# Kernel tuning notes

Hardware: AMD Instinct MI355X
Metric: run time of the kernel (lower is better)

The kernel has to match this reference:

```python
import jax, jax.numpy as jnp
import numpy as np
import math

B, N, D, H, E, EDGE_DIM, GEO_DIM = 32, 256, 512, 8, 1024, 256, 64
HD = D // H

def _lin(x, W, b):
    return x @ W.T + b

def _ln(x, g, b):
    m = x.mean(-1, keepdims=True)
    v = ((x - m) ** 2).mean(-1, keepdims=True)
    return (x - m) * jax.lax.rsqrt(v + 1e-5) * g + b

def setup_inputs() -> dict:
    key = jax.random.key(0)
    ks = jax.random.split(key, 20)
    p = lambda k, s: jax.random.normal(k, s, jnp.float32) * 0.02
    inp = {
        'x': jax.random.normal(ks[0], (B, N, D), jnp.float32),
        'node_masks': jnp.ones((B, N), jnp.float32),
        'relation_edges': jax.random.randint(ks[1], (B, E, 2), 0, N),
        'relation_masks': (jax.random.uniform(ks[2], (B, E)) > 0.2).astype(jnp.float32),
        'relation_embeddings': jax.random.normal(ks[3], (B, E, EDGE_DIM), jnp.float32),
        'relation_geo_features': jax.random.normal(ks[4], (B, E, GEO_DIM), jnp.float32),
        'Wq': p(ks[5], (D, D)), 'bq': jnp.zeros((D,), jnp.float32),
        'Wk': p(ks[6], (D, D)), 'bk': jnp.zeros((D,), jnp.float32),
        'Wv': p(ks[7], (D, D)), 'bv': jnp.zeros((D,), jnp.float32),
        'W_eb': p(ks[8], (H, EDGE_DIM)), 'b_eb': jnp.zeros((H,), jnp.float32),
        'geo_ln_g': jnp.ones((GEO_DIM,), jnp.float32), 'geo_ln_b': jnp.zeros((GEO_DIM,), jnp.float32),
        'W_geo': p(ks[9], (H, GEO_DIM)), 'b_geo': jnp.zeros((H,), jnp.float32),
        'W_out': p(ks[10], (D, D)), 'b_out': jnp.zeros((D,), jnp.float32),
        'norm_g': jnp.ones((D,), jnp.float32), 'norm_b': jnp.zeros((D,), jnp.float32),
        'ff_ln_g': jnp.ones((D,), jnp.float32), 'ff_ln_b': jnp.zeros((D,), jnp.float32),
        'W_ff1': p(ks[11], (4 * D, D)), 'b_ff1': jnp.zeros((4 * D,), jnp.float32),
        'W_ff2': p(ks[12], (D, 4 * D)), 'b_ff2': jnp.zeros((D,), jnp.float32),
    }
    return inp

def reference(x, node_masks, relation_edges, relation_masks, relation_embeddings,
              relation_geo_features, Wq, bq, Wk, bk, Wv, bv, W_eb, b_eb,
              geo_ln_g, geo_ln_b, W_geo, b_geo, W_out, b_out, norm_g, norm_b,
              ff_ln_g, ff_ln_b, W_ff1, b_ff1, W_ff2, b_ff2):
    residual = x
    xn = _ln(x, norm_g, norm_b)
    q = _lin(xn, Wq, bq).reshape(B, N, H, HD)
    k = _lin(xn, Wk, bk).reshape(B, N, H, HD)
    v = _lin(xn, Wv, bv).reshape(B, N, H, HD)
    attn = jnp.einsum('bihd,bjhd->bhij', q, k) / math.sqrt(HD)

    nm = node_masks.astype(bool)
    pair_mask = nm[:, None, :, None] & nm[:, None, None, :]  # [B,1,N,N]

    valid = relation_masks.astype(bool)  # [B,E]
    idx = jnp.clip(relation_edges.astype(jnp.int32), 0, N - 1)
    src, dst = idx[..., 0], idx[..., 1]
    # route invalid edges to padding index N (sliced away after scatter)
    src_w = jnp.where(valid, src, N)
    dst_w = jnp.where(valid, dst, N)
    b_idx = jnp.broadcast_to(jnp.arange(B)[:, None], (B, E))

    adj = jnp.zeros((B, N + 1, N + 1), bool).at[:, :N, :N].set(jnp.eye(N, dtype=bool))
    adj = adj.at[b_idx, src_w, dst_w].set(True).at[b_idx, dst_w, src_w].set(True)
    rel_adj = adj[:, None, :N, :N]  # [B,1,N,N]

    eb = _lin(relation_embeddings, W_eb, b_eb)  # [B,E,H]
    gb = _lin(_ln(relation_geo_features, geo_ln_g, geo_ln_b), W_geo, b_geo)
    total_bias = (eb + gb).transpose(0, 2, 1)  # [B,H,E]
    bb = jnp.broadcast_to(b_idx[:, None, :], (B, H, E))
    hh = jnp.broadcast_to(jnp.arange(H)[None, :, None], (B, H, E))
    ss = jnp.broadcast_to(src_w[:, None, :], (B, H, E))
    dd = jnp.broadcast_to(dst_w[:, None, :], (B, H, E))
    rb = jnp.zeros((B, H, N + 1, N + 1), x.dtype)
    rb = rb.at[bb, hh, ss, dd].set(total_bias).at[bb, hh, dd, ss].set(total_bias)
    attn = attn + rb[:, :, :N, :N]

    mask = pair_mask & rel_adj
    attn = jnp.where(mask, attn, jnp.finfo(attn.dtype).min)
    attn = jnp.nan_to_num(jax.nn.softmax(attn, axis=-1))
    out = jnp.einsum('bhij,bjhd->bihd', attn, v).reshape(B, N, D)
    x2 = residual + _lin(out, W_out, b_out)
    h1 = jax.nn.silu(_lin(_ln(x2, ff_ln_g, ff_ln_b), W_ff1, b_ff1))
    x3 = x2 + _lin(h1, W_ff2, b_ff2)
    return x3 * node_masks[..., None]
```

## Files before the change

kernel.cpp:

```cpp
#include <hip/hip_runtime.h>

#define B_ 32
#define N_ 256
#define D_ 512
#define H_ 8
#define E_ 1024
#define HD_ 64

using u16 = unsigned short;
typedef short bf8_t __attribute__((ext_vector_type(8)));
typedef float f4_t __attribute__((ext_vector_type(4)));

__device__ __forceinline__ u16 f2bf(float f) {
  union { float f; unsigned u; } x; x.f = f;
  unsigned r = x.u + 0x7fffu + ((x.u >> 16) & 1u);
  return (u16)(r >> 16);
}
__device__ __forceinline__ float bf2f(u16 x) {
  union { unsigned u; float f; } y; y.u = ((unsigned)x) << 16; return y.f;
}
__device__ __forceinline__ f4_t mfma16(bf8_t a, bf8_t b, f4_t c) {
  return __builtin_amdgcn_mfma_f32_16x16x32_bf16(a, b, c, 0, 0, 0);
}
__device__ __forceinline__ void gload_lds16(const u16* g, u16* s) {
  __builtin_amdgcn_global_load_lds((const __attribute__((address_space(1))) void*)g,
                                   (__attribute__((address_space(3))) void*)s, 16, 0, 0);
}

__global__ __launch_bounds__(256) void prep_kernel(
    const float* __restrict__ wq, const float* __restrict__ wk,
    const float* __restrict__ wv, const float* __restrict__ wo,
    const float* __restrict__ w1, const float* __restrict__ w2,
    u16* __restrict__ dq, u16* __restrict__ dk, u16* __restrict__ dv,
    u16* __restrict__ dox, u16* __restrict__ d1, u16* __restrict__ d2,
    const float* __restrict__ x, const float* __restrict__ ng,
    const float* __restrict__ nb, u16* __restrict__ xn,
    const int* __restrict__ edges, const float* __restrict__ rmask,
    int* __restrict__ win,
    const float* __restrict__ remb, const float* __restrict__ rgeo,
    const float* __restrict__ Web, const float* __restrict__ beb,
    const float* __restrict__ glng, const float* __restrict__ glnb,
    const float* __restrict__ Wgeo, const float* __restrict__ bgeo,
    float* __restrict__ tb) {
  __shared__ float red[8];
  __shared__ u16 sWeb[16 * 256];
  __shared__ u16 sWgeo[16 * 64];
  __shared__ float sLgb[128];
  const int t = threadIdx.x;
  const int blk0 = blockIdx.x;

  if (blk0 < 3072) {
    int blk = blk0;
    const float* src; u16* dst;
    if (blk < 256)        { src = wq; dst = dq; }
    else if (blk < 512)   { src = wk; dst = dk; blk -= 256; }
    else if (blk < 768)   { src = wv; dst = dv; blk -= 512; }
    else if (blk < 1024)  { src = wo; dst = dox; blk -= 768; }
    else if (blk < 2048)  { src = w1; dst = d1; blk -= 1024; }
    else                  { src = w2; dst = d2; blk -= 2048; }
    const int i = (blk * 256 + t) * 4;
    const float4 v = *(const float4*)(src + i);
    ushort4 o;
    o.x = f2bf(v.x); o.y = f2bf(v.y); o.z = f2bf(v.z); o.w = f2bf(v.w);
    *(ushort4*)(dst + i) = o;
  } else if (blk0 < 11264) {
    const int row = blk0 - 3072;
    const float* xr = x + (size_t)row * D_;
    float v0 = xr[t], v1 = xr[t + 256];
    float s = v0 + v1, ss = v0 * v0 + v1 * v1;
    #pragma unroll
    for (int m = 1; m < 64; m <<= 1) { s += __shfl_xor(s, m, 64); ss += __shfl_xor(ss, m, 64); }
    const int wave = t >> 6, lane = t & 63;
    if (!lane) { red[wave] = s; red[wave + 4] = ss; }
    __syncthreads();
    s = red[0] + red[1] + red[2] + red[3];
    ss = red[4] + red[5] + red[6] + red[7];
    const float mean = s * (1.f / D_);
    const float var = ss * (1.f / D_) - mean * mean;
    const float rs = rsqrtf(var + 1e-5f);
    xn[(size_t)row * D_ + t] = f2bf((v0 - mean) * rs * ng[t] + nb[t]);
    xn[(size_t)row * D_ + t + 256] = f2bf((v1 - mean) * rs * ng[t + 256] + nb[t + 256]);
  } else if (blk0 < 11392) {
    const int idx = (blk0 - 11264) * 256 + t;
    if (rmask[idx] != 0.f) {
      const int b = idx >> 10, e = idx & (E_ - 1);
      int s = edges[2 * idx], d = edges[2 * idx + 1];
      s = min(max(s, 0), N_ - 1);
      d = min(max(d, 0), N_ - 1);
      int* wb = win + (size_t)b * N_ * N_;
      atomicMax(&wb[s * N_ + d], e);
      atomicMax(&wb[d * N_ + s], E_ + e);
    }
  } else {
    const int eblk = blk0 - 11392;
    for (int i = t; i < 2048; i += 256) { sWeb[i] = f2bf(Web[i]); sWeb[2048 + i] = 0; }
    for (int i = t; i < 512; i += 256)  { sWgeo[i] = f2bf(Wgeo[i]); sWgeo[512 + i] = 0; }
    if (t < 64) { sLgb[t] = glng[t]; sLgb[64 + t] = glnb[t]; }
    __syncthreads();
    const int wave = t >> 6, lane = t & 63;
    const int am = lane & 15, quad = lane >> 4;
    const int e0 = eblk * 64 + wave * 16;

    f4_t acc = f4_t{0.f, 0.f, 0.f, 0.f};
    const float* ar = remb + (size_t)(e0 + am) * 256 + quad * 8;
    #pragma unroll
    for (int kt = 0; kt < 256; kt += 32) {
      const float4 p0 = *(const float4*)(ar + kt);
      const float4 p1 = *(const float4*)(ar + kt + 4);
      bf8_t a;
      a[0] = (short)f2bf(p0.x); a[1] = (short)f2bf(p0.y);
      a[2] = (short)f2bf(p0.z); a[3] = (short)f2bf(p0.w);
      a[4] = (short)f2bf(p1.x); a[5] = (short)f2bf(p1.y);
      a[6] = (short)f2bf(p1.z); a[7] = (short)f2bf(p1.w);
      const bf8_t bv = *(const bf8_t*)&sWeb[am * 256 + kt + quad * 8];
      acc = mfma16(a, bv, acc);
    }
    const float* gr = rgeo + (size_t)(e0 + am) * 64;
    float v[16];
    {
      const float4 p0 = *(const float4*)(gr + quad * 8);
      const float4 p1 = *(const float4*)(gr + quad * 8 + 4);
      const float4 p2 = *(const float4*)(gr + 32 + quad * 8);
      const float4 p3 = *(const float4*)(gr + 32 + quad * 8 + 4);
      v[0] = p0.x; v[1] = p0.y; v[2] = p0.z; v[3] = p0.w;
      v[4] = p1.x; v[5] = p1.y; v[6] = p1.z; v[7] = p1.w;
      v[8] = p2.x; v[9] = p2.y; v[10] = p2.z; v[11] = p2.w;
      v[12] = p3.x; v[13] = p3.y; v[14] = p3.z; v[15] = p3.w;
    }
    float s = 0.f, ss = 0.f;
    #pragma unroll
    for (int j = 0; j < 16; ++j) { s += v[j]; ss += v[j] * v[j]; }
    s += __shfl_xor(s, 16, 64);  ss += __shfl_xor(ss, 16, 64);
    s += __shfl_xor(s, 32, 64);  ss += __shfl_xor(ss, 32, 64);
    const float mean = s * (1.f / 64.f);
    const float rs = rsqrtf(ss * (1.f / 64.f) - mean * mean + 1e-5f);
    bf8_t a2, a3;
    #pragma unroll
    for (int j = 0; j < 8; ++j) {
      a2[j] = (short)f2bf((v[j] - mean) * rs * sLgb[quad * 8 + j] + sLgb[64 + quad * 8 + j]);
      a3[j] = (short)f2bf((v[8 + j] - mean) * rs * sLgb[32 + quad * 8 + j] +
                          sLgb[96 + quad * 8 + j]);
    }
    acc = mfma16(a2, *(const bf8_t*)&sWgeo[am * 64 + quad * 8], acc);
    acc = mfma16(a3, *(const bf8_t*)&sWgeo[am * 64 + 32 + quad * 8], acc);
    if (am < 8) {
      const float bias_v = beb[am] + bgeo[am];
      #pragma unroll
      for (int r = 0; r < 4; ++r) {
        const int eg = e0 + quad * 4 + r;
        tb[(size_t)((eg >> 10) * H_ + am) * E_ + (eg & (E_ - 1))] = acc[r] + bias_v;
      }
    }
  }
}

__global__ __launch_bounds__(256) void ln_kernel(const float* __restrict__ x,
                                                 const float* __restrict__ g,
                                                 const float* __restrict__ bta,
                                                 u16* __restrict__ out) {
  const int row = blockIdx.x, t = threadIdx.x;
  const float* xr = x + (size_t)row * D_;
  float v0 = xr[t], v1 = xr[t + 256];
  float s = v0 + v1, ss = v0 * v0 + v1 * v1;
  #pragma unroll
  for (int m = 1; m < 64; m <<= 1) { s += __shfl_xor(s, m, 64); ss += __shfl_xor(ss, m, 64); }
  __shared__ float red[8];
  const int wave = t >> 6, lane = t & 63;
  if (!lane) { red[wave] = s; red[wave + 4] = ss; }
  __syncthreads();
  s = red[0] + red[1] + red[2] + red[3];
  ss = red[4] + red[5] + red[6] + red[7];
  const float mean = s * (1.f / D_);
  const float var = ss * (1.f / D_) - mean * mean;
  const float rs = rsqrtf(var + 1e-5f);
  out[(size_t)row * D_ + t] = f2bf((v0 - mean) * rs * g[t] + bta[t]);
  out[(size_t)row * D_ + t + 256] = f2bf((v1 - mean) * rs * g[t + 256] + bta[t + 256]);
}

__global__ __launch_bounds__(256) void attn_kernel(
    const u16* __restrict__ q, const u16* __restrict__ k, const u16* __restrict__ v,
    const float* __restrict__ tb, const int* __restrict__ win,
    const float* __restrict__ nm, u16* __restrict__ out) {
  const int t = threadIdx.x;
  const int wave = t >> 6, lane = t & 63;
  const int g = blockIdx.x * 4 + wave;
  const int b = g >> 8, row = g & (N_ - 1);
  u16* op = out + (size_t)g * D_ + lane * 8;
  const float nmr = nm[g];
  if (nmr == 0.f) {
    bf8_t z = 0;
    *(bf8_t*)op = z;
    return;
  }
  float qf[8];
  {
    const bf8_t qv = *(const bf8_t*)(q + (size_t)g * D_ + lane * 8);
    #pragma unroll
    for (int j = 0; j < 8; ++j) qf[j] = bf2f((u16)qv[j]);
  }
  int4 w4 = *(const int4*)(win + (size_t)g * N_ + lane * 4);
  if (lane == (row >> 2)) {
    const int sl = row & 3;
    if (sl == 0)      { if (w4.x == -1) w4.x = 0x7FFFFFFF; }
    else if (sl == 1) { if (w4.y == -1) w4.y = 0x7FFFFFFF; }
    else if (sl == 2) { if (w4.z == -1) w4.z = 0x7FFFFFFF; }
    else              { if (w4.w == -1) w4.w = 0x7FFFFFFF; }
  }
  const float* tbh = tb + (size_t)(b * H_ + (lane >> 3)) * E_;
  const float* nmb = nm + b * N_;
  const u16* kb = k + (size_t)b * N_ * D_;
  const u16* vb = v + (size_t)b * N_ * D_;
  float m = -3.402823466e38f, sum = 0.f;
  float o[8];
  #pragma unroll
  for (int j = 0; j < 8; ++j) o[j] = 0.f;
  #pragma unroll
  for (int c = 0; c < 4; ++c) {
    const int wc = (c == 0) ? w4.x : (c == 1) ? w4.y : (c == 2) ? w4.z : w4.w;
    unsigned long long mk = __ballot(wc != -1);
    while (mk) {
      const int jl = __builtin_ctzll(mk);
      mk &= mk - 1;
      const int col = jl * 4 + c;
      const int wv = __shfl(wc, jl, 64);
      const float nmc = nmb[col];
      if (nmc == 0.f) continue;
      const bf8_t kv = *(const bf8_t*)(kb + (size_t)col * D_ + lane * 8);
      float d = 0.f;
      #pragma unroll
      for (int j = 0; j < 8; ++j) d += qf[j] * bf2f((u16)kv[j]);
      d += __shfl_xor(d, 1, 64);
      d += __shfl_xor(d, 2, 64);
      d += __shfl_xor(d, 4, 64);
      float s = d * 0.125f;
      if ((unsigned)wv < 2048u) s += tbh[wv & (E_ - 1)];
      const bf8_t vv = *(const bf8_t*)(vb + (size_t)col * D_ + lane * 8);
      if (s > m) {
        const float sc = __expf(m - s);
        sum *= sc;
        #pragma unroll
        for (int j = 0; j < 8; ++j) o[j] *= sc;
        m = s;
      }
      const float p = __expf(s - m);
      sum += p;
      #pragma unroll
      for (int j = 0; j < 8; ++j) o[j] += p * bf2f((u16)vv[j]);
    }
  }
  const float rinv = 1.f / sum;
  bf8_t res;
  #pragma unroll
  for (int j = 0; j < 8; ++j) res[j] = (short)f2bf(o[j] * rinv);
  *(bf8_t*)op = res;
}

template <int MODE, int BN>
__global__ __launch_bounds__(256, 2) void gemm_k(
    const u16* __restrict__ A,
    const u16* __restrict__ W0, const u16* __restrict__ W1, const u16* __restrict__ W2,
    const float* __restrict__ b0, const float* __restrict__ b1, const float* __restrict__ b2,
    void* d0, void* d1, void* d2,
    const void* res, const float* __restrict__ nmask, int K) {
  constexpr int MJ = BN / 32;
  constexpr int CB = BN / 32;
  __shared__ u16 As[128 * 64];
  __shared__ u16 Bs[BN * 64];
  const int tid = threadIdx.x;
  const int wave = tid >> 6, lane = tid & 63;
  const int am = lane & 15, quad = lane >> 4;
  const int m0 = blockIdx.x * 128;
  int n0, proj = 0;
  const u16* W;
  const float* bias;
  if constexpr (MODE == 0) {
    constexpr int NPB = 512 / BN;
    proj = blockIdx.y / NPB;
    n0 = (blockIdx.y % NPB) * BN;
    W = proj == 0 ? W0 : (proj == 1 ? W1 : W2);
    bias = proj == 0 ? b0 : (proj == 1 ? b1 : b2);
  } else {
    n0 = blockIdx.y * BN;
    W = W0;
    bias = b0;
  }
  const int wm = (wave >> 1) * 64;
  const int wn = (wave & 1) * (BN / 2);

  f4_t acc[4][MJ];
  #pragma unroll
  for (int i = 0; i < 4; ++i)
    #pragma unroll
    for (int j = 0; j < MJ; ++j) acc[i][j] = f4_t{0.f, 0.f, 0.f, 0.f};

  int arow[4], aq[4], brow[CB], bq[CB];
  #pragma unroll
  for (int c = 0; c < 4; ++c) {
    const int g = (wave * 4 + c) * 64 + lane;
    arow[c] = g >> 3;
    aq[c] = (g & 7) ^ (arow[c] & 7);
  }
  #pragma unroll
  for (int c = 0; c < CB; ++c) {
    const int g = (wave * CB + c) * 64 + lane;
    brow[c] = g >> 3;
    bq[c] = (g & 7) ^ (brow[c] & 7);
  }

  for (int kt = 0; kt < K; kt += 64) {
    #pragma unroll
    for (int c = 0; c < 4; ++c)
      gload_lds16(A + (size_t)(m0 + arow[c]) * K + kt + aq[c] * 8, &As[(wave * 4 + c) * 512]);
    #pragma unroll
    for (int c = 0; c < CB; ++c)
      gload_lds16(W + (size_t)(n0 + brow[c]) * K + kt + bq[c] * 8, &Bs[(wave * CB + c) * 512]);
    __syncthreads();
    #pragma unroll
    for (int kc = 0; kc < 2; ++kc) {
      bf8_t af[4], bfv[MJ];
      #pragma unroll
      for (int i = 0; i < 4; ++i) {
        const int r = wm + i * 16 + am;
        af[i] = *(const bf8_t*)&As[r * 64 + (((kc * 4 + quad) ^ (r & 7)) * 8)];
      }
      #pragma unroll
      for (int j = 0; j < MJ; ++j) {
        const int r = wn + j * 16 + am;
        bfv[j] = *(const bf8_t*)&Bs[r * 64 + (((kc * 4 + quad) ^ (r & 7)) * 8)];
      }
      #pragma unroll
      for (int i = 0; i < 4; ++i)
        #pragma unroll
        for (int j = 0; j < MJ; ++j)
          acc[i][j] = mfma16(bfv[j], af[i], acc[i][j]);
    }
    __syncthreads();
  }

  const int row0 = m0 + wm + am;
  const int col0 = n0 + wn + quad * 4;
  #pragma unroll
  for (int j = 0; j < MJ; ++j) {
    const int col = col0 + j * 16;
    const float4 bv4 = *(const float4*)(bias + col);
    #pragma unroll
    for (int i = 0; i < 4; ++i) {
      const int row = row0 + i * 16;
      float v0 = acc[i][j][0] + bv4.x;
      float v1 = acc[i][j][1] + bv4.y;
      float v2 = acc[i][j][2] + bv4.z;
      float v3 = acc[i][j][3] + bv4.w;
      if constexpr (MODE == 0) {
        u16* dst = (u16*)(proj == 0 ? d0 : (proj == 1 ? d1 : d2));
        ushort4 o; o.x = f2bf(v0); o.y = f2bf(v1); o.z = f2bf(v2); o.w = f2bf(v3);
        *(ushort4*)(dst + (size_t)row * D_ + col) = o;
      } else if constexpr (MODE == 2) {
        const float4 rr = *(const float4*)((const float*)res + (size_t)row * D_ + col);
        float4 o; o.x = v0 + rr.x; o.y = v1 + rr.y; o.z = v2 + rr.z; o.w = v3 + rr.w;
        *(float4*)((float*)d0 + (size_t)row * D_ + col) = o;
      } else if constexpr (MODE == 3) {
        v0 = v0 / (1.f + __expf(-v0));
        v1 = v1 / (1.f + __expf(-v1));
        v2 = v2 / (1.f + __expf(-v2));
        v3 = v3 / (1.f + __expf(-v3));
        ushort4 o; o.x = f2bf(v0); o.y = f2bf(v1); o.z = f2bf(v2); o.w = f2bf(v3);
        *(ushort4*)((u16*)d0 + (size_t)row * 2048 + col) = o;
      } else {
        const float4 rr = *(const float4*)((const float*)res + (size_t)row * D_ + col);
        const float nmv = nmask[row];
        float4 o;
        o.x = (v0 + rr.x) * nmv; o.y = (v1 + rr.y) * nmv;
        o.z = (v2 + rr.z) * nmv; o.w = (v3 + rr.w) * nmv;
        *(float4*)((float*)d0 + (size_t)row * D_ + col) = o;
      }
    }
  }
}

extern "C" void kernel_launch(void* const* d_in, const int* in_sizes, int n_in,
                              void* d_out, int out_size, void* d_ws, size_t ws_size,
                              hipStream_t stream) {
  const float* x     = (const float*)d_in[0];
  const float* nm    = (const float*)d_in[1];
  const int*   edges = (const int*)d_in[2];
  const float* rmask = (const float*)d_in[3];
  const float* remb  = (const float*)d_in[4];
  const float* rgeo  = (const float*)d_in[5];
  const float* Wq = (const float*)d_in[6];  const float* bq = (const float*)d_in[7];
  const float* Wk = (const float*)d_in[8];  const float* bk = (const float*)d_in[9];
  const float* Wv = (const float*)d_in[10]; const float* bv = (const float*)d_in[11];
  const float* Web = (const float*)d_in[12]; const float* beb = (const float*)d_in[13];
  const float* glng = (const float*)d_in[14]; const float* glnb = (const float*)d_in[15];
  const float* Wgeo = (const float*)d_in[16]; const float* bgeo = (const float*)d_in[17];
  const float* Wout = (const float*)d_in[18]; const float* bout = (const float*)d_in[19];
  const float* ng = (const float*)d_in[20]; const float* nb = (const float*)d_in[21];
  const float* fg = (const float*)d_in[22]; const float* fb = (const float*)d_in[23];
  const float* Wff1 = (const float*)d_in[24]; const float* bff1 = (const float*)d_in[25];
  const float* Wff2 = (const float*)d_in[26]; const float* bff2 = (const float*)d_in[27];

  char* ws = (char*)d_ws;
  u16*   xn      = (u16*)(ws + 0);
  u16*   qb      = (u16*)(ws + 8388608);
  u16*   kb      = (u16*)(ws + 16777216);
  u16*   vb      = (u16*)(ws + 25165824);
  u16*   h1      = (u16*)(ws + 0);
  int*   win     = (int*)(ws + 33554432);
  u16*   x2n     = (u16*)(ws + 33554432);
  float* tb      = (float*)(ws + 41943040);
  u16* Wq16   = (u16*)(ws + 42991616);
  u16* Wk16   = (u16*)(ws + 43515904);
  u16* Wv16   = (u16*)(ws + 44040192);
  u16* Wout16 = (u16*)(ws + 44564480);
  u16* Wff116 = (u16*)(ws + 45088768);
  u16* Wff216 = (u16*)(ws + 47185920);
  u16*   attnout = xn;
  float* out     = (float*)d_out;

  hipMemsetAsync(win, 0xFF, (size_t)B_ * N_ * N_ * sizeof(int), stream);
  prep_kernel<<<11904, 256, 0, stream>>>(
      Wq, Wk, Wv, Wout, Wff1, Wff2, Wq16, Wk16, Wv16, Wout16, Wff116, Wff216,
      x, ng, nb, xn,
      edges, rmask, win,
      remb, rgeo, Web, beb, glng, glnb, Wgeo, bgeo, tb);
  gemm_k<0, 128><<<dim3(64, 12), 256, 0, stream>>>(xn, Wq16, Wk16, Wv16, bq, bk, bv,
                                                   (void*)qb, (void*)kb, (void*)vb,
                                                   nullptr, nullptr, D_);
  attn_kernel<<<dim3(B_ * N_ / 4), 256, 0, stream>>>(qb, kb, vb, tb, win, nm, attnout);
  gemm_k<2, 64><<<dim3(64, 8), 256, 0, stream>>>(attnout, Wout16, nullptr, nullptr,
                                                 bout, nullptr, nullptr,
                                                 (void*)out, nullptr, nullptr,
                                                 (const void*)x, nullptr, D_);
  ln_kernel<<<B_ * N_, 256, 0, stream>>>(out, fg, fb, x2n);
  gemm_k<3, 128><<<dim3(64, 16), 256, 0, stream>>>(x2n, Wff116, nullptr, nullptr,
                                                   bff1, nullptr, nullptr,
                                                   (void*)h1, nullptr, nullptr, nullptr, nullptr, D_);
  gemm_k<4, 64><<<dim3(64, 8), 256, 0, stream>>>(h1, Wff216, nullptr, nullptr,
                                                 bff2, nullptr, nullptr,
                                                 (void*)out, nullptr, nullptr,
                                                 (const void*)out, nm, 2048);
}
```

Measured before the change: 291.7 us.

## Double-buffer GEMM LDS tiles to overlap global loads with MFMA compute

The GEMM kernel now keeps two LDS buffers for the A and W tiles. It prefetches the next K-tile with direct-to-LDS loads while MFMAs run on the current one, using explicit vmcnt waits and raw s_barrier in place of __syncthreads. This is meant to hide global load latency behind compute. In exchange, LDS use doubles, which may limit occupancy under the 2-blocks launch bound. The hand-counted vmcnt values must also match the number of outstanding loads, or the kernel reads stale data.

```diff
diff --git a/kernel.cpp b/kernel.cpp
--- a/kernel.cpp
+++ b/kernel.cpp
@@ -264,8 +264,8 @@
     const void* res, const float* __restrict__ nmask, int K) {
   constexpr int MJ = BN / 32;
   constexpr int CB = BN / 32;
-  __shared__ u16 As[128 * 64];
-  __shared__ u16 Bs[BN * 64];
+  __shared__ u16 As[2][128 * 64];
+  __shared__ u16 Bs[2][BN * 64];
   const int tid = threadIdx.x;
   const int wave = tid >> 6, lane = tid & 63;
   const int am = lane & 15, quad = lane >> 4;
@@ -307,26 +307,43 @@
     bq[c] = (g & 7) ^ (brow[c] & 7);
   }
 
+  #pragma unroll
+  for (int c = 0; c < 4; ++c)
+    gload_lds16(A + (size_t)(m0 + arow[c]) * K + aq[c] * 8, &As[0][(wave * 4 + c) * 512]);
+  #pragma unroll
+  for (int c = 0; c < CB; ++c)
+    gload_lds16(W + (size_t)(n0 + brow[c]) * K + bq[c] * 8, &Bs[0][(wave * CB + c) * 512]);
+
+  int cur = 0;
   for (int kt = 0; kt < K; kt += 64) {
-    #pragma unroll
-    for (int c = 0; c < 4; ++c)
-      gload_lds16(A + (size_t)(m0 + arow[c]) * K + kt + aq[c] * 8, &As[(wave * 4 + c) * 512]);
-    #pragma unroll
-    for (int c = 0; c < CB; ++c)
-      gload_lds16(W + (size_t)(n0 + brow[c]) * K + kt + bq[c] * 8, &Bs[(wave * CB + c) * 512]);
-    __syncthreads();
+    const int nxt = cur ^ 1;
+    if (kt + 64 < K) {
+      #pragma unroll
+      for (int c = 0; c < 4; ++c)
+        gload_lds16(A + (size_t)(m0 + arow[c]) * K + (kt + 64) + aq[c] * 8,
+                    &As[nxt][(wave * 4 + c) * 512]);
+      #pragma unroll
+      for (int c = 0; c < CB; ++c)
+        gload_lds16(W + (size_t)(n0 + brow[c]) * K + (kt + 64) + bq[c] * 8,
+                    &Bs[nxt][(wave * CB + c) * 512]);
+      if constexpr (BN == 128) asm volatile("s_waitcnt vmcnt(8)" ::: "memory");
+      else                     asm volatile("s_waitcnt vmcnt(6)" ::: "memory");
+    } else {
+      asm volatile("s_waitcnt vmcnt(0)" ::: "memory");
+    }
+    asm volatile("s_barrier" ::: "memory");
     #pragma unroll
     for (int kc = 0; kc < 2; ++kc) {
       bf8_t af[4], bfv[MJ];
       #pragma unroll
       for (int i = 0; i < 4; ++i) {
         const int r = wm + i * 16 + am;
-        af[i] = *(const bf8_t*)&As[r * 64 + (((kc * 4 + quad) ^ (r & 7)) * 8)];
+        af[i] = *(const bf8_t*)&As[cur][r * 64 + (((kc * 4 + quad) ^ (r & 7)) * 8)];
       }
       #pragma unroll
       for (int j = 0; j < MJ; ++j) {
         const int r = wn + j * 16 + am;
-        bfv[j] = *(const bf8_t*)&Bs[r * 64 + (((kc * 4 + quad) ^ (r & 7)) * 8)];
+        bfv[j] = *(const bf8_t*)&Bs[cur][r * 64 + (((kc * 4 + quad) ^ (r & 7)) * 8)];
       }
       #pragma unroll
       for (int i = 0; i < 4; ++i)
@@ -334,7 +351,8 @@
         for (int j = 0; j < MJ; ++j)
           acc[i][j] = mfma16(bfv[j], af[i], acc[i][j]);
     }
-    __syncthreads();
+    asm volatile("s_barrier" ::: "memory");
+    cur = nxt;
   }
 
   const int row0 = m0 + wm + am;
```

New measurement: 300.4 us. 1.03x slower.
